# Optimization experiments

Measured on AMD Instinct MI355X. Metric: run time of the kernel, lower is better.

## Reference

```python
import jax, jax.numpy as jnp
import numpy as np
import math

B, S, D, NS, K, V = 4, 1024, 256, 64, 16, 32000
NEG = -10000.0


def l2n(x, axis=-1):
    # F.normalize with eps=1e-12
    return x / jnp.maximum(jnp.linalg.norm(x, axis=axis, keepdims=True), 1e-12)


def sparsemax(z, axis=-1):
    # sort descending, find support size k_z, threshold tau
    z_sorted = -jnp.sort(-z, axis=axis)
    cumsum = jnp.cumsum(z_sorted, axis=axis)
    n = z.shape[axis]
    k = jnp.arange(1, n + 1, dtype=z.dtype).reshape((1,) * (z.ndim - 1) + (n,))
    check = (1.0 + k * z_sorted > cumsum).astype(z.dtype)
    k_z = jnp.sum(check, axis=axis, keepdims=True)
    tau = (jnp.take_along_axis(cumsum, (k_z - 1).astype(jnp.int32), axis=axis) - 1.0) / k_z
    return jnp.maximum(z - tau, 0.0)


def router_forward(messages, hidden, x_ids, scn, mask, static_nb, geo_velocity,
                   ctx_conf, current_entropy, vel_proj_w, edge_w1, edge_b1,
                   edge_w2, edge_b2, probe_w, geo_gate_w, geo_gate_b):
    S_ = messages.shape[1]
    dg = jnp.eye(S_, dtype=bool)
    mfull = mask[None] | dg[None]  # masked_fill(mask) + diagonal fill combined

    # --- geodesic-endpoint routed attention ---
    endpoint = l2n(scn + 0.4 * geo_velocity)                      # [B,S,NS]
    endpoint_sim = jnp.einsum('bsn,btn->bst', endpoint, scn)      # [B,S,S]
    endpoint_sim = jnp.where(mfull, NEG, endpoint_sim)
    H_norm = jax.lax.stop_gradient(current_entropy)[..., None] / (math.log(V) + 1e-8)
    vel_h = geo_velocity @ vel_proj_w.T                           # [B,S,D]
    h_aimed = l2n(hidden + 0.3 * vel_h)
    h_msg_sim = jnp.einsum('bsd,btd->bst', h_aimed, messages)
    combined_geo = (endpoint_sim * H_norm + 0.5 * h_msg_sim) * 5.0
    combined_geo = jnp.where(mfull, NEG, combined_geo)
    ew_geo = sparsemax(combined_geo, axis=-1)
    geo_agg = jnp.einsum('bst,btd->bsd', ew_geo, messages)

    # --- vocab-neighbor match / aggregate ---
    nb_vocab = static_nb[x_ids]                                   # [B,S,K]
    match = (x_ids[:, None, None, :] == nb_vocab[..., None]).astype(messages.dtype)  # [B,S,K,S]
    causal = jnp.tril(jnp.ones((S_, S_), messages.dtype))
    match = match * causal[None, :, None, :]
    coverage = jnp.mean(jnp.minimum(jnp.sum(match, -1), 1.0), axis=-1, keepdims=True)  # [B,S,1]
    nb_msgs_s = jnp.einsum('bskp,bpd->bskd', match, messages)
    nb_scn_s = jnp.einsum('bskp,bpn->bskn', match, scn)
    sim_s = jnp.sum(nb_scn_s * scn[:, :, None, :], -1)            # [B,S,K]
    e = jax.nn.gelu(sim_s[..., None] @ edge_w1.T + edge_b1, approximate=False)
    e = (e @ edge_w2.T + edge_b2)[..., 0]
    ew_s = jax.nn.softmax(e, axis=-1)
    static_agg = jnp.sum(nb_msgs_s * ew_s[..., None], axis=2)     # [B,S,D]

    # --- local same-mode routing with sparsemax ---
    my_mode = jnp.argmax(scn, -1)
    same_mode = (my_mode[:, :, None] == my_mode[:, None, :]).astype(messages.dtype)
    same_mode = jnp.where(mfull, 0.0, same_mode)
    scn_sim = jnp.einsum('bsn,btn->bst', scn, scn) * same_mode
    has_nb = jnp.sum(same_mode, -1, keepdims=True) > 0
    pos = jnp.arange(S_, dtype=messages.dtype)
    pos_sim = -jnp.abs(pos[:, None] - pos[None, :])[None]
    pos_sim = jnp.where(mfull, NEG, pos_sim)
    routing_sim = jnp.where(has_nb, scn_sim, pos_sim * 0.01)
    routing_sim = jnp.where(mfull, NEG, routing_sim)
    ew_l = sparsemax(routing_sim * 5.0, axis=-1)
    local_agg = jnp.einsum('bst,btd->bsd', ew_l, messages)

    static_final = coverage * static_agg + (1.0 - coverage) * local_agg
    raw_gate = jax.nn.sigmoid(hidden @ geo_gate_w.T + geo_gate_b)
    geo_weight = raw_gate * ctx_conf
    agg = geo_weight * geo_agg + (1.0 - geo_weight) * static_final
    probe = l2n(hidden @ probe_w.T)
    agg_n = l2n(agg)
    rel = jax.nn.sigmoid(jnp.sum(agg_n * probe, -1, keepdims=True))
    return agg * rel


def setup_inputs() -> dict:
    key = jax.random.key(0)
    ks = jax.random.split(key, 14)
    messages = jax.random.normal(ks[0], (B, S, D), jnp.float32)
    hidden = jax.random.normal(ks[1], (B, S, D), jnp.float32)
    x_ids = jax.random.randint(ks[2], (B, S), 0, V)
    scn = jax.random.normal(ks[3], (B, S, NS), jnp.float32)
    mask = ~jnp.tril(jnp.ones((S, S), bool))  # True above diagonal (disallowed)
    static_nb = jax.random.randint(ks[4], (V, K), 0, V)
    geo_velocity = jax.random.normal(ks[5], (B, S, NS), jnp.float32) * 0.5
    ctx_conf = jax.random.uniform(ks[6], (B, S, 1), jnp.float32)
    current_entropy = jax.random.uniform(ks[7], (B, S), jnp.float32) * math.log(V)
    vel_proj_w = jax.random.normal(ks[8], (D, NS), jnp.float32) / np.sqrt(NS).astype(np.float32)
    edge_w1 = jax.random.normal(ks[9], (8, 1), jnp.float32)
    edge_b1 = jnp.zeros((8,), jnp.float32)
    edge_w2 = jax.random.normal(ks[10], (1, 8), jnp.float32) * 0.3
    edge_b2 = jnp.zeros((1,), jnp.float32)
    probe_w = jax.random.normal(ks[11], (D, D), jnp.float32) / np.sqrt(D).astype(np.float32)
    geo_gate_w = jax.random.normal(ks[12], (1, D), jnp.float32) * 0.02
    geo_gate_b = jnp.full((1,), -4.0, jnp.float32)
    return dict(messages=messages, hidden=hidden, x_ids=x_ids, scn=scn, mask=mask,
                static_nb=static_nb, geo_velocity=geo_velocity, ctx_conf=ctx_conf,
                current_entropy=current_entropy, vel_proj_w=vel_proj_w,
                edge_w1=edge_w1, edge_b1=edge_b1, edge_w2=edge_w2, edge_b2=edge_b2,
                probe_w=probe_w, geo_gate_w=geo_gate_w, geo_gate_b=geo_gate_b)


def reference(messages, hidden, x_ids, scn, mask, static_nb, geo_velocity, ctx_conf,
              current_entropy, vel_proj_w, edge_w1, edge_b1, edge_w2, edge_b2,
              probe_w, geo_gate_w, geo_gate_b):
    return router_forward(messages, hidden, x_ids, scn, mask, static_nb, geo_velocity,
                          ctx_conf, current_entropy, vel_proj_w, edge_w1, edge_b1,
                          edge_w2, edge_b2, probe_w, geo_gate_w, geo_gate_b)
```

## Files before the change

kernel.cpp:

```cpp
#include <hip/hip_runtime.h>
#include <math.h>

#define B_ 4
#define S_ 1024
#define D_ 256
#define NS_ 64
#define KNB 16
#define KPACK 320
#define NEG_ (-10000.0f)
#define LOGV_INV (1.0f/(10.373491181781864f + 1e-8f))
#define MCAP 64
#define NCHUNK 16
#define SUPCAP 1024
#define SMC 128

typedef __attribute__((ext_vector_type(8))) short short8;
typedef __attribute__((ext_vector_type(8))) unsigned short ushort8v;
typedef __attribute__((ext_vector_type(4))) float f32x4;


__device__ __forceinline__ void blockReduceSum4(float4& v, float* red) {
  #pragma unroll
  for (int off = 32; off > 0; off >>= 1) {
    v.x += __shfl_down(v.x, off, 64);
    v.y += __shfl_down(v.y, off, 64);
    v.z += __shfl_down(v.z, off, 64);
    v.w += __shfl_down(v.w, off, 64);
  }
  int lane = threadIdx.x & 63;
  int w = threadIdx.x >> 6;
  __syncthreads();
  if (lane == 0) {
    red[w] = v.x; red[4 + w] = v.y; red[8 + w] = v.z; red[12 + w] = v.w;
  }
  __syncthreads();
  v.x = red[0] + red[1] + red[2] + red[3];
  v.y = red[4] + red[5] + red[6] + red[7];
  v.z = red[8] + red[9] + red[10] + red[11];
  v.w = red[12] + red[13] + red[14] + red[15];
}

__device__ __forceinline__ void waveAllSum2(float& a, float& b) {
  #pragma unroll
  for (int off = 1; off < 64; off <<= 1) {
    a += __shfl_xor(a, off, 64);
    b += __shfl_xor(b, off, 64);
  }
}

__device__ __forceinline__ float michelot_tau16(const float* z) {
  float m = z[0];
  #pragma unroll
  for (int k = 1; k < 16; k++) m = fmaxf(m, z[k]);
  #pragma unroll
  for (int off = 1; off < 64; off <<= 1) m = fmaxf(m, __shfl_xor(m, off, 64));
  float thr = m - 1.0f;
  float s = 0.f, c = 0.f;
  #pragma unroll
  for (int k = 0; k < 16; k++) { float zk = z[k]; if (zk > thr) { s += zk; c += 1.f; } }
  waveAllSum2(s, c);
  int cnt = (int)c;
  float tau = (s - 1.0f) / c;
  for (int it = 0; it < 32; ++it) {
    float s2 = 0.f, c2 = 0.f;
    #pragma unroll
    for (int k = 0; k < 16; k++) { float zk = z[k]; if (zk > tau) { s2 += zk; c2 += 1.f; } }
    waveAllSum2(s2, c2);
    int ci = (int)c2;
    if (ci == cnt || ci == 0) break;
    cnt = ci;
    tau = (s2 - 1.0f) / c2;
  }
  return tau;
}

__device__ __forceinline__ unsigned short f2bf_rne(float f) {
  union { float f; unsigned u; } v; v.f = f;
  unsigned r = v.u + 0x7FFFu + ((v.u >> 16) & 1u);
  return (unsigned short)(r >> 16);
}
__device__ __forceinline__ float bf2f(unsigned short h) {
  union { unsigned u; float f; } v; v.u = ((unsigned)h) << 16;
  return v.f;
}
__device__ __forceinline__ void cvt_store4(unsigned short* hi, unsigned short* lo, float4 v) {
  unsigned short h0 = f2bf_rne(v.x), h1 = f2bf_rne(v.y), h2 = f2bf_rne(v.z), h3 = f2bf_rne(v.w);
  *(ushort4*)hi = make_ushort4(h0, h1, h2, h3);
  *(ushort4*)lo = make_ushort4(f2bf_rne(v.x - bf2f(h0)), f2bf_rne(v.y - bf2f(h1)),
                               f2bf_rne(v.z - bf2f(h2)), f2bf_rne(v.w - bf2f(h3)));
}
#define MFMA16(a,b,c) __builtin_amdgcn_mfma_f32_16x16x32_bf16((a),(b),(c),0,0,0)


__global__ __launch_bounds__(256) void bf16_split_kernel(
    const float* __restrict__ messages, const float* __restrict__ hidden,
    const float* __restrict__ scn, const float* __restrict__ gv,
    const float* __restrict__ probe_w, const float* __restrict__ vel_w,
    unsigned short* __restrict__ msg_hi, unsigned short* __restrict__ msg_lo,
    unsigned short* __restrict__ hid_hi, unsigned short* __restrict__ hid_lo,
    unsigned short* __restrict__ scn_hi, unsigned short* __restrict__ scn_lo,
    unsigned short* __restrict__ gv_hi,  unsigned short* __restrict__ gv_lo,
    unsigned short* __restrict__ pw_hi,  unsigned short* __restrict__ pw_lo,
    unsigned short* __restrict__ vw_hi,  unsigned short* __restrict__ vw_lo)
{
  const float* src; unsigned short *hi, *lo; int n;
  switch (blockIdx.y) {
    case 0: src = messages; hi = msg_hi; lo = msg_lo; n = B_*S_*D_;  break;
    case 1: src = hidden;   hi = hid_hi; lo = hid_lo; n = B_*S_*D_;  break;
    case 2: src = scn;      hi = scn_hi; lo = scn_lo; n = B_*S_*NS_; break;
    case 3: src = gv;       hi = gv_hi;  lo = gv_lo;  n = B_*S_*NS_; break;
    case 4: src = probe_w;  hi = pw_hi;  lo = pw_lo;  n = D_*D_;     break;
    default: src = vel_w;   hi = vw_hi;  lo = vw_lo;  n = D_*NS_;    break;
  }
  int idx = (blockIdx.x * 256 + threadIdx.x) * 4;
  if (idx >= n) return;
  float4 v = *(const float4*)(src + idx);
  cvt_store4(hi + idx, lo + idx, v);
}


__global__ __launch_bounds__(256) void msum_partial_kernel(
    const float* __restrict__ messages, float* __restrict__ part)
{
  int blk = blockIdx.x;
  int b = blk >> 4, c = blk & 15;
  int d = threadIdx.x;
  const float* src = messages + ((size_t)b * S_ + c * 64) * D_ + d;
  float acc = 0.f;
  #pragma unroll 8
  for (int t = 0; t < 64; t++) acc += src[t * D_];
  part[((size_t)b * NCHUNK + c) * D_ + d] = acc;
}

#define LDB 40


__global__ __launch_bounds__(256) void dual_gemm_mfma_kernel(
    const unsigned short* __restrict__ hid_hi, const unsigned short* __restrict__ hid_lo,
    const unsigned short* __restrict__ gv_hi,  const unsigned short* __restrict__ gv_lo,
    const unsigned short* __restrict__ pw_hi,  const unsigned short* __restrict__ pw_lo,
    const unsigned short* __restrict__ vw_hi,  const unsigned short* __restrict__ vw_lo,
    float* __restrict__ probe_raw, float* __restrict__ vel_h)
{
  __shared__ unsigned short Ahi[64][LDB], Alo[64][LDB];
  __shared__ unsigned short Bhi[64][LDB], Blo[64][LDB];
  int which = blockIdx.y;
  const unsigned short* Ah = which ? gv_hi : hid_hi;
  const unsigned short* Al = which ? gv_lo : hid_lo;
  const unsigned short* Wh = which ? vw_hi : pw_hi;
  const unsigned short* Wl = which ? vw_lo : pw_lo;
  float* C = which ? vel_h : probe_raw;
  int K = which ? NS_ : D_;

  int mt = blockIdx.x >> 2, nt4 = blockIdx.x & 3;
  int s0 = mt * 64, t0 = nt4 * 64;
  int tid = threadIdx.x, lane = tid & 63, w = tid >> 6;
  int fm = lane & 15, fq = lane >> 4;
  int si = tid >> 2, sc = tid & 3;

  f32x4 acc[4];
  #pragma unroll
  for (int i = 0; i < 4; i++) acc[i] = (f32x4){0.f, 0.f, 0.f, 0.f};

  ushort8v rAh, rAl, rBh, rBl;
  rAh = *(const ushort8v*)(Ah + (size_t)(s0 + si) * K + 0 + sc*8);
  rAl = *(const ushort8v*)(Al + (size_t)(s0 + si) * K + 0 + sc*8);
  rBh = *(const ushort8v*)(Wh + (size_t)(t0 + si) * K + 0 + sc*8);
  rBl = *(const ushort8v*)(Wl + (size_t)(t0 + si) * K + 0 + sc*8);

  for (int k0 = 0; k0 < K; k0 += 32) {
    __syncthreads();
    *(ushort8v*)&Ahi[si][sc*8] = rAh;
    *(ushort8v*)&Alo[si][sc*8] = rAl;
    *(ushort8v*)&Bhi[si][sc*8] = rBh;
    *(ushort8v*)&Blo[si][sc*8] = rBl;
    __syncthreads();
    int kn = k0 + 32;
    if (kn < K) {
      rAh = *(const ushort8v*)(Ah + (size_t)(s0 + si) * K + kn + sc*8);
      rAl = *(const ushort8v*)(Al + (size_t)(s0 + si) * K + kn + sc*8);
      rBh = *(const ushort8v*)(Wh + (size_t)(t0 + si) * K + kn + sc*8);
      rBl = *(const ushort8v*)(Wl + (size_t)(t0 + si) * K + kn + sc*8);
    }
    short8 ah = *(const short8*)&Ahi[w*16 + fm][fq*8];
    short8 al = *(const short8*)&Alo[w*16 + fm][fq*8];
    #pragma unroll
    for (int nt = 0; nt < 4; nt++) {
      short8 bh = *(const short8*)&Bhi[nt*16 + fm][fq*8];
      short8 bl = *(const short8*)&Blo[nt*16 + fm][fq*8];
      acc[nt] = MFMA16(ah, bh, acc[nt]);
      acc[nt] = MFMA16(ah, bl, acc[nt]);
      acc[nt] = MFMA16(al, bh, acc[nt]);
    }
  }

  #pragma unroll
  for (int nt = 0; nt < 4; nt++)
    #pragma unroll
    for (int rg = 0; rg < 4; rg++)
      C[(size_t)(s0 + w*16 + fq*4 + rg) * D_ + t0 + nt*16 + fm] = acc[nt][rg];
}


__global__ __launch_bounds__(256) void prep3_kernel(
    const float* __restrict__ hidden,
    const float* __restrict__ scn, const float* __restrict__ gv,
    const float* __restrict__ ctx_conf, const float* __restrict__ entropy,
    const float* __restrict__ probe_raw, const float* __restrict__ vel_h,
    const float* __restrict__ gate_w, const float* __restrict__ gate_b,
    unsigned short* __restrict__ arow_hi, unsigned short* __restrict__ arow_lo,
    float* __restrict__ probe, float* __restrict__ gw_out,
    int* __restrict__ mode_out)
{
  int r = blockIdx.x;
  int tid = threadIdx.x;
  __shared__ float sh_scn[NS_];
  __shared__ float red[16];

  float sv = 0.f, gvv = 0.f;
  if (tid < NS_) {
    sv  = scn[(size_t)r*NS_ + tid];
    gvv = gv[(size_t)r*NS_ + tid];
    sh_scn[tid] = sv;
  }
  float hid = hidden[(size_t)r*D_ + tid];
  float vh  = vel_h[(size_t)r*D_ + tid];
  float pr  = probe_raw[(size_t)r*D_ + tid];
  float gwt = gate_w[tid];

  float ep = (tid < NS_) ? (sv + 0.4f*gvv) : 0.f;
  float ha = hid + 0.3f*vh;

  float4 v = make_float4(ep*ep, ha*ha, pr*pr, hid*gwt);
  blockReduceSum4(v, red);

  float Hn = entropy[r] * LOGV_INV;
  float epn = fmaxf(sqrtf(v.x), 1e-12f);
  float han = fmaxf(sqrtf(v.y), 1e-12f);
  float prn = fmaxf(sqrtf(v.z), 1e-12f);

  if (tid < NS_) {
    float v0 = (5.0f*Hn) * (ep / epn);
    unsigned short h = f2bf_rne(v0);
    arow_hi[(size_t)r*KPACK + tid] = h;
    arow_lo[(size_t)r*KPACK + tid] = f2bf_rne(v0 - bf2f(h));
  }
  {
    float v1 = 2.5f * (ha / han);
    unsigned short h = f2bf_rne(v1);
    arow_hi[(size_t)r*KPACK + NS_ + tid] = h;
    arow_lo[(size_t)r*KPACK + NS_ + tid] = f2bf_rne(v1 - bf2f(h));
  }
  probe[(size_t)r*D_ + tid] = pr / prn;

  if (tid == 0) {
    float rg = 1.f/(1.f + expf(-(v.w + gate_b[0])));
    gw_out[r] = rg * ctx_conf[r];
    float m = sh_scn[0]; int mi = 0;
    for (int n = 1; n < NS_; n++) { if (sh_scn[n] > m) { m = sh_scn[n]; mi = n; } }
    mode_out[r] = mi;
  }
}


#define GBT 64
#define GBK 32
#define NTRI 136

__global__ __launch_bounds__(256) void geo_gemm_mfma2_kernel(
    const unsigned short* __restrict__ arow_hi, const unsigned short* __restrict__ arow_lo,
    const unsigned short* __restrict__ scn_hi,  const unsigned short* __restrict__ scn_lo,
    const unsigned short* __restrict__ msg_hi,  const unsigned short* __restrict__ msg_lo,
    float* __restrict__ z, float* __restrict__ sim)
{
  __shared__ unsigned short Ahi[GBT][LDB], Alo[GBT][LDB];
  __shared__ unsigned short Bhi[GBT][LDB], Blo[GBT][LDB];
  __shared__ unsigned short A2hi[GBT][LDB], A2lo[GBT][LDB];

  int blk = blockIdx.x;
  int b = blk / NTRI;
  int tri = blk % NTRI;
  int ts = 0;
  while ((ts + 1) * (ts + 2) / 2 <= tri) ts++;
  int tt = tri - ts * (ts + 1) / 2;
  int s0 = ts * GBT, t0 = tt * GBT;

  const unsigned short* Ah = arow_hi + (size_t)b * S_ * KPACK;
  const unsigned short* Al = arow_lo + (size_t)b * S_ * KPACK;
  const unsigned short* Sh = scn_hi + (size_t)b * S_ * NS_;
  const unsigned short* Sl = scn_lo + (size_t)b * S_ * NS_;
  const unsigned short* Mh = msg_hi + (size_t)b * S_ * D_;
  const unsigned short* Ml = msg_lo + (size_t)b * S_ * D_;

  int tid = threadIdx.x, lane = tid & 63, w = tid >> 6;
  int fm = lane & 15, fq = lane >> 4;
  int si = tid >> 2, sc = tid & 3;

  f32x4 accz[4], accs[4];
  #pragma unroll
  for (int i = 0; i < 4; i++) {
    accz[i] = (f32x4){0.f, 0.f, 0.f, 0.f};
    accs[i] = (f32x4){0.f, 0.f, 0.f, 0.f};
  }

  ushort8v rAh, rAl, rBh, rBl, rA2h, rA2l;
  {
    rAh  = *(const ushort8v*)(Ah + (size_t)(s0 + si) * KPACK + 0 + sc*8);
    rAl  = *(const ushort8v*)(Al + (size_t)(s0 + si) * KPACK + 0 + sc*8);
    rBh  = *(const ushort8v*)(Sh + (size_t)(t0 + si) * NS_ + 0 + sc*8);
    rBl  = *(const ushort8v*)(Sl + (size_t)(t0 + si) * NS_ + 0 + sc*8);
    rA2h = *(const ushort8v*)(Sh + (size_t)(s0 + si) * NS_ + 0 + sc*8);
    rA2l = *(const ushort8v*)(Sl + (size_t)(s0 + si) * NS_ + 0 + sc*8);
  }

  for (int k0 = 0; k0 < KPACK; k0 += GBK) {
    bool scn_slab = (k0 < NS_);
    __syncthreads();
    *(ushort8v*)&Ahi[si][sc*8] = rAh;
    *(ushort8v*)&Alo[si][sc*8] = rAl;
    *(ushort8v*)&Bhi[si][sc*8] = rBh;
    *(ushort8v*)&Blo[si][sc*8] = rBl;
    if (scn_slab) {
      *(ushort8v*)&A2hi[si][sc*8] = rA2h;
      *(ushort8v*)&A2lo[si][sc*8] = rA2l;
    }
    __syncthreads();

    int kn = k0 + GBK;
    if (kn < KPACK) {
      bool next_scn = (kn < NS_);
      rAh = *(const ushort8v*)(Ah + (size_t)(s0 + si) * KPACK + kn + sc*8);
      rAl = *(const ushort8v*)(Al + (size_t)(s0 + si) * KPACK + kn + sc*8);
      if (next_scn) {
        rBh  = *(const ushort8v*)(Sh + (size_t)(t0 + si) * NS_ + kn + sc*8);
        rBl  = *(const ushort8v*)(Sl + (size_t)(t0 + si) * NS_ + kn + sc*8);
        rA2h = *(const ushort8v*)(Sh + (size_t)(s0 + si) * NS_ + kn + sc*8);
        rA2l = *(const ushort8v*)(Sl + (size_t)(s0 + si) * NS_ + kn + sc*8);
      } else {
        rBh = *(const ushort8v*)(Mh + (size_t)(t0 + si) * D_ + (kn - NS_) + sc*8);
        rBl = *(const ushort8v*)(Ml + (size_t)(t0 + si) * D_ + (kn - NS_) + sc*8);
      }
    }

    short8 ah = *(const short8*)&Ahi[w*16 + fm][fq*8];
    short8 al = *(const short8*)&Alo[w*16 + fm][fq*8];
    short8 a2h, a2l;
    if (scn_slab) {
      a2h = *(const short8*)&A2hi[w*16 + fm][fq*8];
      a2l = *(const short8*)&A2lo[w*16 + fm][fq*8];
    }
    #pragma unroll
    for (int nt = 0; nt < 4; nt++) {
      short8 bh = *(const short8*)&Bhi[nt*16 + fm][fq*8];
      short8 bl = *(const short8*)&Blo[nt*16 + fm][fq*8];
      accz[nt] = MFMA16(ah, bh, accz[nt]);
      accz[nt] = MFMA16(ah, bl, accz[nt]);
      accz[nt] = MFMA16(al, bh, accz[nt]);
      if (scn_slab) {
        accs[nt] = MFMA16(a2h, bh, accs[nt]);
        accs[nt] = MFMA16(a2h, bl, accs[nt]);
        accs[nt] = MFMA16(a2l, bh, accs[nt]);
      }
    }
  }

  float* zb = z + (size_t)b * S_ * S_;
  float* sb = sim + (size_t)b * S_ * S_;
  #pragma unroll
  for (int nt = 0; nt < 4; nt++) {
    #pragma unroll
    for (int rg = 0; rg < 4; rg++) {
      int row = s0 + w*16 + fq*4 + rg;
      int col = t0 + nt*16 + fm;
      zb[(size_t)row * S_ + col] = accz[nt][rg];
      sb[(size_t)row * S_ + col] = accs[nt][rg];
    }
  }
}


__global__ __launch_bounds__(256) void rows_fused10_kernel(
    const float* __restrict__ zbuf, const float* __restrict__ simbuf,
    const float* __restrict__ messages, const int* __restrict__ mode,
    const int* __restrict__ x_ids, const int* __restrict__ static_nb,
    const float* __restrict__ ew1, const float* __restrict__ eb1,
    const float* __restrict__ ew2, const float* __restrict__ eb2,
    const float* __restrict__ gw, const float* __restrict__ probe,
    const float* __restrict__ part, float* __restrict__ out)
{
  __shared__ int xb_l[S_];
  __shared__ int mode_l[S_];
  __shared__ unsigned short gt_l[2][SUPCAP];
  __shared__ float gw_l[2][SUPCAP];
  __shared__ unsigned short lt_l[2][SUPCAP];
  __shared__ float lw_l[2][SUPCAP];
  __shared__ unsigned short sm_l[2][SMC];
  __shared__ int gcnt_s[2], lcnt_s[2], smcnt_s[2];
  __shared__ float taul_s[2];
  __shared__ unsigned short mk_s[2][MCAP];
  __shared__ unsigned short mp_s[2][MCAP];
  __shared__ float ews[2][KNB];
  __shared__ float cov_s[2];
  __shared__ int M_s[2];
  __shared__ float red2[2][2][2];

  const int tid = threadIdx.x;
  const int lane = tid & 63;
  const int wv = tid >> 6;
  const int rw = wv >> 1;
  const int half = wv & 1;
  const int r = blockIdx.x * 2 + rw;
  const int b = r >> 10, s = r & 1023;
  const unsigned long long lmask_lt = (1ull << lane) - 1ull;

  const float2* msg2 = (const float2*)(messages + (size_t)b * S_ * D_);
  const int dbase = half * 64 + lane;

  ((int4*)xb_l)[tid]   = ((const int4*)(x_ids + (size_t)b * S_))[tid];
  ((int4*)mode_l)[tid] = ((const int4*)(mode + (size_t)b * S_))[tid];
  __syncthreads();

  if (half == 0) {
    if (s != 0) {
      const float4* zrow4 = (const float4*)(zbuf + (size_t)r * S_);
      float zg[16];
      #pragma unroll
      for (int j = 0; j < 4; j++) {
        int t0 = j*256 + lane*4;
        if (j*256 < s) {
          float4 v = zrow4[j*64 + lane];
          zg[j*4+0] = (t0+0 < s) ? v.x : NEG_;
          zg[j*4+1] = (t0+1 < s) ? v.y : NEG_;
          zg[j*4+2] = (t0+2 < s) ? v.z : NEG_;
          zg[j*4+3] = (t0+3 < s) ? v.w : NEG_;
        } else {
          zg[j*4+0] = NEG_; zg[j*4+1] = NEG_; zg[j*4+2] = NEG_; zg[j*4+3] = NEG_;
        }
      }
      float tau = michelot_tau16(zg);
      int base = 0;
      #pragma unroll
      for (int k = 0; k < 16; k++) {
        float w = zg[k] - tau;
        bool p = w > 0.f;
        unsigned long long m = __ballot(p);
        if (p) {
          int idx = base + __popcll(m & lmask_lt);
          gt_l[rw][idx] = (unsigned short)((k >> 2)*256 + lane*4 + (k & 3));
          gw_l[rw][idx] = w;
        }
        base += __popcll(m);
      }
      if (lane == 0) gcnt_s[rw] = base;
    } else if (lane == 0) gcnt_s[rw] = 0;

    int xid = xb_l[s];
    int nb[KNB];
    #pragma unroll
    for (int k = 0; k < KNB; k++) nb[k] = static_nb[(size_t)xid * KNB + k];
    float simk[KNB];
    #pragma unroll
    for (int k = 0; k < KNB; k++) simk[k] = 0.f;
    unsigned int kmask = 0;
    int M = 0;
    for (int j = 0; j < 16; j++) {
      int p = j*64 + lane;
      int xp = xb_l[p];
      bool anym = false;
      #pragma unroll
      for (int k = 0; k < KNB; k++) anym |= (nb[k] == xp);
      anym = anym && (p <= s);
      float d_self = 0.f;
      if (anym) d_self = simbuf[(size_t)r * S_ + p];
      unsigned long long m = __ballot(anym);
      while (m) {
        int ln = __ffsll((unsigned long long)m) - 1; m &= m - 1;
        int pp = j*64 + ln;
        int xpp = xb_l[pp];
        float d = __shfl(d_self, ln, 64);
        #pragma unroll
        for (int k = 0; k < KNB; k++) {
          if (nb[k] == xpp) {
            if (M < MCAP && lane == 0) { mk_s[rw][M] = (unsigned short)k; mp_s[rw][M] = (unsigned short)pp; }
            M++;
            simk[k] += d;
            kmask |= (1u << k);
          }
        }
      }
    }
    if (M > MCAP) M = MCAP;
    if (lane == 0) { M_s[rw] = M; cov_s[rw] = (float)__popc(kmask) * (1.0f/(float)KNB); }
    if (M > 0) {
      if (lane == 0) {
        #pragma unroll
        for (int k = 0; k < KNB; k++) ews[rw][k] = simk[k];
      }
      float sim = (lane < KNB) ? ews[rw][lane] : 0.f;
      float e = eb2[0];
      #pragma unroll
      for (int j = 0; j < 8; j++) {
        float x = sim * ew1[j] + eb1[j];
        float gx = 0.5f * x * (1.0f + erff(x * 0.70710678118654752f));
        e += gx * ew2[j];
      }
      float mx = e;
      #pragma unroll
      for (int off = 1; off < 16; off <<= 1) mx = fmaxf(mx, __shfl_xor(mx, off, 64));
      float ex = expf(e - mx);
      float ssum = ex;
      #pragma unroll
      for (int off = 1; off < 16; off <<= 1) ssum += __shfl_xor(ssum, off, 64);
      if (lane < KNB) ews[rw][lane] = ex / ssum;
    }
  } else {
    if (s != 0) {
      int mode_s = mode_l[s];
      int smcnt = 0;
      unsigned int pmask = 0;
      #pragma unroll
      for (int j = 0; j < 16; j++) {
        int t = j*64 + lane;
        bool p = (t < s) && (mode_l[t] == mode_s);
        unsigned long long m = __ballot(p);
        if (p) {
          pmask |= (1u << j);
          int idx = smcnt + __popcll(m & lmask_lt);
          if (idx < SMC) sm_l[rw][idx] = (unsigned short)t;
        }
        smcnt += __popcll(m);
      }
      bool has_nb = smcnt > 0;
      if (lane == 0) smcnt_s[rw] = smcnt;
      float zl[16];
      #pragma unroll
      for (int j = 0; j < 16; j++) {
        int t = j*64 + lane;
        float zv;
        if (t >= s) zv = NEG_ * 5.0f;
        else if (pmask & (1u << j)) zv = simbuf[(size_t)r * S_ + t] * 5.0f;
        else if (has_nb) zv = 0.f;
        else zv = (0.01f * (-(float)(s - t))) * 5.0f;
        zl[j] = zv;
      }
      float tau = michelot_tau16(zl);
      if (lane == 0) taul_s[rw] = tau;
      int base = 0;
      #pragma unroll
      for (int j = 0; j < 16; j++) {
        float w = zl[j] - tau;
        bool p = w > 0.f;
        unsigned long long m = __ballot(p);
        if (p) {
          int idx = base + __popcll(m & lmask_lt);
          lt_l[rw][idx] = (unsigned short)(j*64 + lane);
          lw_l[rw][idx] = w;
        }
        base += __popcll(m);
      }
      if (lane == 0) lcnt_s[rw] = base;
    } else if (lane == 0) { lcnt_s[rw] = 0; smcnt_s[rw] = 0; }
  }
  __syncthreads();

  float2 accg = {0.f, 0.f}, accl = {0.f, 0.f}, accs = {0.f, 0.f};
  const float2* part2 = (const float2*)(part + (size_t)b * NCHUNK * D_);
  if (s == 0) {
    float2 msum = {0.f, 0.f};
    #pragma unroll
    for (int c = 0; c < NCHUNK; c++) {
      float2 pm = part2[c * 128 + dbase];
      msum.x += pm.x; msum.y += pm.y;
    }
    accg.x = 0.0009765625f * msum.x; accg.y = 0.0009765625f * msum.y;
    accl.x = 0.00390625f * msum.x;   accl.y = 0.00390625f * msum.y;
  } else {
    int gc = gcnt_s[rw];
    for (int i = 0; i < gc; i++) {
      float w = gw_l[rw][i];
      float2 mm = msg2[(size_t)gt_l[rw][i] * 128 + dbase];
      accg.x += w*mm.x; accg.y += w*mm.y;
    }
    int lc = lcnt_s[rw];
    int smc = smcnt_s[rw];
    if (lc >= 256 && smc >= 1 && smc <= SMC) {
      float taul = taul_s[rw];
      float w0 = -taul;
      float2 psum = {0.f, 0.f};
      int nc = s >> 6;
      for (int c = 0; c < nc; c++) {
        float2 pm = part2[c * 128 + dbase];
        psum.x += pm.x; psum.y += pm.y;
      }
      for (int t = nc * 64; t < s; t++) {
        float2 mm = msg2[(size_t)t * 128 + dbase];
        psum.x += mm.x; psum.y += mm.y;
      }
      accl.x = w0 * psum.x; accl.y = w0 * psum.y;
      const float* simrow = simbuf + (size_t)r * S_;
      for (int i = 0; i < smc; i++) {
        int t = sm_l[rw][i];
        float sv5 = simrow[t] * 5.0f;
        float corr = (sv5 - taul > 0.f) ? sv5 : taul;
        float2 mm = msg2[(size_t)t * 128 + dbase];
        accl.x += corr * mm.x; accl.y += corr * mm.y;
      }
    } else {
      for (int i = 0; i < lc; i++) {
        float w = lw_l[rw][i];
        float2 mm = msg2[(size_t)lt_l[rw][i] * 128 + dbase];
        accl.x += w*mm.x; accl.y += w*mm.y;
      }
    }
  }
  {
    int M = M_s[rw];
    for (int i = 0; i < M; i++) {
      int k = mk_s[rw][i], p = mp_s[rw][i];
      float w = ews[rw][k];
      float2 mm = msg2[(size_t)p * 128 + dbase];
      accs.x += w*mm.x; accs.y += w*mm.y;
    }
  }

  float g = gw[r];
  float cov = cov_s[rw];
  float2 agg;
  agg.x = g*accg.x + (1.f-g)*(cov*accs.x + (1.f-cov)*accl.x);
  agg.y = g*accg.y + (1.f-g)*(cov*accs.y + (1.f-cov)*accl.y);

  float2 pv = ((const float2*)probe)[(size_t)r * 128 + dbase];
  float n2 = agg.x*agg.x + agg.y*agg.y;
  float ap = agg.x*pv.x + agg.y*pv.y;
  waveAllSum2(n2, ap);
  if (lane == 0) { red2[rw][half][0] = n2; red2[rw][half][1] = ap; }
  __syncthreads();
  n2 = red2[rw][0][0] + red2[rw][1][0];
  ap = red2[rw][0][1] + red2[rw][1][1];
  float nrm = fmaxf(sqrtf(n2), 1e-12f);
  float rel = 1.f / (1.f + expf(-(ap / nrm)));
  float2 o;
  o.x = agg.x * rel; o.y = agg.y * rel;
  ((float2*)out)[(size_t)r * 128 + dbase] = o;
}


extern "C" void kernel_launch(void* const* d_in, const int* in_sizes, int n_in,
                              void* d_out, int out_size, void* d_ws, size_t ws_size,
                              hipStream_t stream)
{
  const float* messages  = (const float*)d_in[0];
  const float* hidden    = (const float*)d_in[1];
  const int*   x_ids     = (const int*)d_in[2];
  const float* scn       = (const float*)d_in[3];
  const int*   static_nb = (const int*)d_in[5];
  const float* gv        = (const float*)d_in[6];
  const float* ctx_conf  = (const float*)d_in[7];
  const float* entropy   = (const float*)d_in[8];
  const float* vel_w     = (const float*)d_in[9];
  const float* ew1       = (const float*)d_in[10];
  const float* eb1       = (const float*)d_in[11];
  const float* ew2       = (const float*)d_in[12];
  const float* eb2       = (const float*)d_in[13];
  const float* probe_w   = (const float*)d_in[14];
  const float* gate_w    = (const float*)d_in[15];
  const float* gate_b    = (const float*)d_in[16];
  float* out = (float*)d_out;

  float* ws = (float*)d_ws;
  float* probe   = ws;
  float* gwbuf   = probe + (size_t)B_*S_*D_;
  int*   mode    = (int*)(gwbuf + (size_t)B_*S_);
  float* zbuf    = (float*)(mode + (size_t)B_*S_);
  float* simbuf  = zbuf + (size_t)B_*S_*S_;
  float* vel_h   = simbuf + (size_t)B_*S_*S_;
  float* part    = vel_h + (size_t)B_*S_*D_;
  unsigned short* msg_hi  = (unsigned short*)(part + (size_t)B_*NCHUNK*D_);
  unsigned short* msg_lo  = msg_hi  + (size_t)B_*S_*D_;
  unsigned short* scn_hi  = msg_lo  + (size_t)B_*S_*D_;
  unsigned short* scn_lo  = scn_hi  + (size_t)B_*S_*NS_;
  unsigned short* arow_hi = scn_lo  + (size_t)B_*S_*NS_;
  unsigned short* arow_lo = arow_hi + (size_t)B_*S_*KPACK;
  unsigned short* hid_hi = (unsigned short*)zbuf;
  unsigned short* hid_lo = hid_hi + (size_t)B_*S_*D_;
  unsigned short* gv_hi  = hid_lo + (size_t)B_*S_*D_;
  unsigned short* gv_lo  = gv_hi  + (size_t)B_*S_*NS_;
  unsigned short* pw_hi  = gv_lo  + (size_t)B_*S_*NS_;
  unsigned short* pw_lo  = pw_hi  + (size_t)D_*D_;
  unsigned short* vw_hi  = pw_lo  + (size_t)D_*D_;
  unsigned short* vw_lo  = vw_hi  + (size_t)D_*NS_;

  bf16_split_kernel<<<dim3(1024, 6), dim3(256), 0, stream>>>(
      messages, hidden, scn, gv, probe_w, vel_w,
      msg_hi, msg_lo, hid_hi, hid_lo, scn_hi, scn_lo,
      gv_hi, gv_lo, pw_hi, pw_lo, vw_hi, vw_lo);

  msum_partial_kernel<<<dim3(B_*NCHUNK), dim3(256), 0, stream>>>(messages, part);

  dual_gemm_mfma_kernel<<<dim3(256, 2), dim3(256), 0, stream>>>(
      hid_hi, hid_lo, gv_hi, gv_lo, pw_hi, pw_lo, vw_hi, vw_lo,
      probe, vel_h);

  prep3_kernel<<<dim3(B_*S_), dim3(256), 0, stream>>>(
      hidden, scn, gv, ctx_conf, entropy, probe, vel_h,
      gate_w, gate_b, arow_hi, arow_lo, probe, gwbuf, mode);

  geo_gemm_mfma2_kernel<<<dim3(B_*NTRI), dim3(256), 0, stream>>>(
      arow_hi, arow_lo, scn_hi, scn_lo, msg_hi, msg_lo, zbuf, simbuf);

  rows_fused10_kernel<<<dim3(B_*S_/2), dim3(256), 0, stream>>>(
      zbuf, simbuf, messages, mode, x_ids, static_nb,
      ew1, eb1, ew2, eb2, gwbuf, probe, part, out);
}
```

Measured before the change: 166.8 us.

## Shrink support-list LDS buffers with recompute fallback, fold msum into split kernel

The per-row sparsemax support lists in LDS shrink from 1024 to 320 entries. This cuts shared memory per block and should let more blocks stay resident on each CU. When a support set overflows the cap, the kernel falls back to rescanning the z or sim row against the stored threshold. Separately, the message partial-sum kernel becomes an extra grid slice of the bf16 split kernel, removing one launch. Rows with large supports now take slower scan paths, and the local fallback rebuilds the z values from mode and sim data, which adds a risk of mismatch.

```diff
diff --git a/kernel.cpp b/kernel.cpp
--- a/kernel.cpp
+++ b/kernel.cpp
@@ -11,7 +11,7 @@
 #define LOGV_INV (1.0f/(10.373491181781864f + 1e-8f))
 #define MCAP 64
 #define NCHUNK 16
-#define SUPCAP 1024
+#define LCAP 320
 #define SMC 128
 
 typedef __attribute__((ext_vector_type(8))) short short8;
@@ -92,7 +92,7 @@
 #define MFMA16(a,b,c) __builtin_amdgcn_mfma_f32_16x16x32_bf16((a),(b),(c),0,0,0)
 
 
-__global__ __launch_bounds__(256) void bf16_split_kernel(
+__global__ __launch_bounds__(256) void split_msum_kernel(
     const float* __restrict__ messages, const float* __restrict__ hidden,
     const float* __restrict__ scn, const float* __restrict__ gv,
     const float* __restrict__ probe_w, const float* __restrict__ vel_w,
@@ -101,8 +101,21 @@
     unsigned short* __restrict__ scn_hi, unsigned short* __restrict__ scn_lo,
     unsigned short* __restrict__ gv_hi,  unsigned short* __restrict__ gv_lo,
     unsigned short* __restrict__ pw_hi,  unsigned short* __restrict__ pw_lo,
-    unsigned short* __restrict__ vw_hi,  unsigned short* __restrict__ vw_lo)
+    unsigned short* __restrict__ vw_hi,  unsigned short* __restrict__ vw_lo,
+    float* __restrict__ part)
 {
+  if (blockIdx.y == 6) {
+    int blk = blockIdx.x;
+    if (blk >= B_ * NCHUNK) return;
+    int b = blk >> 4, c = blk & 15;
+    int d = threadIdx.x;
+    const float* src = messages + ((size_t)b * S_ + c * 64) * D_ + d;
+    float acc = 0.f;
+    #pragma unroll 8
+    for (int t = 0; t < 64; t++) acc += src[t * D_];
+    part[((size_t)b * NCHUNK + c) * D_ + d] = acc;
+    return;
+  }
   const float* src; unsigned short *hi, *lo; int n;
   switch (blockIdx.y) {
     case 0: src = messages; hi = msg_hi; lo = msg_lo; n = B_*S_*D_;  break;
@@ -116,20 +129,6 @@
   if (idx >= n) return;
   float4 v = *(const float4*)(src + idx);
   cvt_store4(hi + idx, lo + idx, v);
-}
-
-
-__global__ __launch_bounds__(256) void msum_partial_kernel(
-    const float* __restrict__ messages, float* __restrict__ part)
-{
-  int blk = blockIdx.x;
-  int b = blk >> 4, c = blk & 15;
-  int d = threadIdx.x;
-  const float* src = messages + ((size_t)b * S_ + c * 64) * D_ + d;
-  float acc = 0.f;
-  #pragma unroll 8
-  for (int t = 0; t < 64; t++) acc += src[t * D_];
-  part[((size_t)b * NCHUNK + c) * D_ + d] = acc;
 }
 
 #define LDB 40
@@ -379,7 +378,7 @@
 }
 
 
-__global__ __launch_bounds__(256) void rows_fused10_kernel(
+__global__ __launch_bounds__(256) void rows_fused11_kernel(
     const float* __restrict__ zbuf, const float* __restrict__ simbuf,
     const float* __restrict__ messages, const int* __restrict__ mode,
     const int* __restrict__ x_ids, const int* __restrict__ static_nb,
@@ -390,13 +389,13 @@
 {
   __shared__ int xb_l[S_];
   __shared__ int mode_l[S_];
-  __shared__ unsigned short gt_l[2][SUPCAP];
-  __shared__ float gw_l[2][SUPCAP];
-  __shared__ unsigned short lt_l[2][SUPCAP];
-  __shared__ float lw_l[2][SUPCAP];
+  __shared__ unsigned short gt_l[2][LCAP];
+  __shared__ float gw_l[2][LCAP];
+  __shared__ unsigned short lt_l[2][LCAP];
+  __shared__ float lw_l[2][LCAP];
   __shared__ unsigned short sm_l[2][SMC];
   __shared__ int gcnt_s[2], lcnt_s[2], smcnt_s[2];
-  __shared__ float taul_s[2];
+  __shared__ float taug_s[2], taul_s[2];
   __shared__ unsigned short mk_s[2][MCAP];
   __shared__ unsigned short mp_s[2][MCAP];
   __shared__ float ews[2][KNB];
@@ -438,6 +437,7 @@
         }
       }
       float tau = michelot_tau16(zg);
+      if (lane == 0) taug_s[rw] = tau;
       int base = 0;
       #pragma unroll
       for (int k = 0; k < 16; k++) {
@@ -446,8 +446,7 @@
         unsigned long long m = __ballot(p);
         if (p) {
           int idx = base + __popcll(m & lmask_lt);
-          gt_l[rw][idx] = (unsigned short)((k >> 2)*256 + lane*4 + (k & 3));
-          gw_l[rw][idx] = w;
+          if (idx < LCAP) { gt_l[rw][idx] = (unsigned short)((k >> 2)*256 + lane*4 + (k & 3)); gw_l[rw][idx] = w; }
         }
         base += __popcll(m);
       }
@@ -553,8 +552,7 @@
         unsigned long long m = __ballot(p);
         if (p) {
           int idx = base + __popcll(m & lmask_lt);
-          lt_l[rw][idx] = (unsigned short)(j*64 + lane);
-          lw_l[rw][idx] = w;
+          if (idx < LCAP) { lt_l[rw][idx] = (unsigned short)(j*64 + lane); lw_l[rw][idx] = w; }
         }
         base += __popcll(m);
       }
@@ -576,14 +574,32 @@
     accl.x = 0.00390625f * msum.x;   accl.y = 0.00390625f * msum.y;
   } else {
     int gc = gcnt_s[rw];
-    for (int i = 0; i < gc; i++) {
-      float w = gw_l[rw][i];
-      float2 mm = msg2[(size_t)gt_l[rw][i] * 128 + dbase];
-      accg.x += w*mm.x; accg.y += w*mm.y;
+    if (gc <= LCAP) {
+      for (int i = 0; i < gc; i++) {
+        float w = gw_l[rw][i];
+        float2 mm = msg2[(size_t)gt_l[rw][i] * 128 + dbase];
+        accg.x += w*mm.x; accg.y += w*mm.y;
+      }
+    } else {
+      float taug = taug_s[rw];
+      const float* zrow = zbuf + (size_t)r * S_;
+      for (int t = 0; t < s; t++) {
+        float w = zrow[t] - taug;
+        if (w > 0.f) {
+          float2 mm = msg2[(size_t)t * 128 + dbase];
+          accg.x += w*mm.x; accg.y += w*mm.y;
+        }
+      }
     }
     int lc = lcnt_s[rw];
     int smc = smcnt_s[rw];
-    if (lc >= 256 && smc >= 1 && smc <= SMC) {
+    if (lc <= LCAP) {
+      for (int i = 0; i < lc; i++) {
+        float w = lw_l[rw][i];
+        float2 mm = msg2[(size_t)lt_l[rw][i] * 128 + dbase];
+        accl.x += w*mm.x; accl.y += w*mm.y;
+      }
+    } else if (smc >= 1 && smc <= SMC) {
       float taul = taul_s[rw];
       float w0 = -taul;
       float2 psum = {0.f, 0.f};
@@ -606,10 +622,20 @@
         accl.x += corr * mm.x; accl.y += corr * mm.y;
       }
     } else {
-      for (int i = 0; i < lc; i++) {
-        float w = lw_l[rw][i];
-        float2 mm = msg2[(size_t)lt_l[rw][i] * 128 + dbase];
-        accl.x += w*mm.x; accl.y += w*mm.y;
+      float taul = taul_s[rw];
+      bool has_nb = smc > 0;
+      int mode_s = mode_l[s];
+      const float* simrow = simbuf + (size_t)r * S_;
+      for (int t = 0; t < s; t++) {
+        float zv;
+        if (mode_l[t] == mode_s) zv = simrow[t] * 5.0f;
+        else if (has_nb) zv = 0.f;
+        else zv = (0.01f * (-(float)(s - t))) * 5.0f;
+        float w = zv - taul;
+        if (w > 0.f) {
+          float2 mm = msg2[(size_t)t * 128 + dbase];
+          accl.x += w*mm.x; accl.y += w*mm.y;
+        }
       }
     }
   }
@@ -690,12 +716,10 @@
   unsigned short* vw_hi  = pw_lo  + (size_t)D_*D_;
   unsigned short* vw_lo  = vw_hi  + (size_t)D_*NS_;
 
-  bf16_split_kernel<<<dim3(1024, 6), dim3(256), 0, stream>>>(
+  split_msum_kernel<<<dim3(1024, 7), dim3(256), 0, stream>>>(
       messages, hidden, scn, gv, probe_w, vel_w,
       msg_hi, msg_lo, hid_hi, hid_lo, scn_hi, scn_lo,
-      gv_hi, gv_lo, pw_hi, pw_lo, vw_hi, vw_lo);
-
-  msum_partial_kernel<<<dim3(B_*NCHUNK), dim3(256), 0, stream>>>(messages, part);
+      gv_hi, gv_lo, pw_hi, pw_lo, vw_hi, vw_lo, part);
 
   dual_gemm_mfma_kernel<<<dim3(256, 2), dim3(256), 0, stream>>>(
       hid_hi, hid_lo, gv_hi, gv_lo, pw_hi, pw_lo, vw_hi, vw_lo,
@@ -708,7 +732,7 @@
   geo_gemm_mfma2_kernel<<<dim3(B_*NTRI), dim3(256), 0, stream>>>(
       arow_hi, arow_lo, scn_hi, scn_lo, msg_hi, msg_lo, zbuf, simbuf);
 
-  rows_fused10_kernel<<<dim3(B_*S_/2), dim3(256), 0, stream>>>(
+  rows_fused11_kernel<<<dim3(B_*S_/2), dim3(256), 0, stream>>>(
       zbuf, simbuf, messages, mode, x_ids, static_nb,
       ew1, eb1, ew2, eb2, gwbuf, probe, part, out);
 }
```

Result: faster. 162.8 us (-2.3%).
